# Optimization experiments

Hardware: AMD Instinct MI355X
Metric: run time of the kernel (lower is better)

The kernel has to match this reference:

```python
import jax, jax.numpy as jnp
import numpy as np

N = 100000      # nodes
E = 1600000     # edges
F_IN = 64       # num_node_features
HID = 128       # hidden_channels
HEADS = 8       # heads in gat1
G = 1000        # number of graphs
EPS = 1e-5


def _layer_norm(x, gamma, beta):
    mu = jnp.mean(x, axis=-1, keepdims=True)
    var = jnp.var(x, axis=-1, keepdims=True)
    return (x - mu) * jax.lax.rsqrt(var + EPS) * gamma + beta


def _gat_conv(x, src, dst, W, a_src, a_dst, b):
    # PyG GATConv (concat=True, negative_slope=0.2, self-loops already in src/dst)
    n = x.shape[0]
    heads, c = a_src.shape
    h = (x @ W).reshape(n, heads, c)                      # [N,H,C]
    alpha_s = jnp.sum(h * a_src[None], axis=-1)           # [N,H]
    alpha_d = jnp.sum(h * a_dst[None], axis=-1)           # [N,H]
    e = jax.nn.leaky_relu(alpha_s[src] + alpha_d[dst], 0.2)   # [Etot,H]
    m = jax.ops.segment_max(e, dst, num_segments=n)       # per-dst max (stable softmax)
    e = jnp.exp(e - m[dst])
    denom = jax.ops.segment_sum(e, dst, num_segments=n)
    attn = e / (denom[dst] + 1e-16)                        # [Etot,H]
    out = jax.ops.segment_sum(h[src] * attn[:, :, None], dst, num_segments=n)
    return out.reshape(n, heads * c) + b


def setup_inputs():
    key = jax.random.key(0)
    ks = jax.random.split(key, 32)
    s = 0.05
    inp = {
        'x': jax.random.normal(ks[0], (N, F_IN), dtype=jnp.float32),
        'edge_index': jax.random.randint(ks[1], (2, E), 0, N),
        'batch': jnp.sort(jax.random.randint(ks[2], (N,), 0, G)),
        # gat1: 64 -> 16 per head, 8 heads
        'W1': jax.random.normal(ks[3], (F_IN, HID), dtype=jnp.float32) * s,
        'as1': jax.random.normal(ks[4], (HEADS, HID // HEADS), dtype=jnp.float32) * s,
        'ad1': jax.random.normal(ks[5], (HEADS, HID // HEADS), dtype=jnp.float32) * s,
        'b1': jnp.zeros((HID,), dtype=jnp.float32),
        # gat2: 128 -> 128, 1 head
        'W2': jax.random.normal(ks[6], (HID, HID), dtype=jnp.float32) * s,
        'as2': jax.random.normal(ks[7], (1, HID), dtype=jnp.float32) * s,
        'ad2': jax.random.normal(ks[8], (1, HID), dtype=jnp.float32) * s,
        'b2': jnp.zeros((HID,), dtype=jnp.float32),
        # gat3
        'W3': jax.random.normal(ks[9], (HID, HID), dtype=jnp.float32) * s,
        'as3': jax.random.normal(ks[10], (1, HID), dtype=jnp.float32) * s,
        'ad3': jax.random.normal(ks[11], (1, HID), dtype=jnp.float32) * s,
        'b3': jnp.zeros((HID,), dtype=jnp.float32),
        # layer norms
        'g1': jnp.ones((HID,), dtype=jnp.float32), 'be1': jnp.zeros((HID,), dtype=jnp.float32),
        'g2': jnp.ones((HID,), dtype=jnp.float32), 'be2': jnp.zeros((HID,), dtype=jnp.float32),
        'g3': jnp.ones((HID,), dtype=jnp.float32), 'be3': jnp.zeros((HID,), dtype=jnp.float32),
        # linear heads
        'lw1': jax.random.normal(ks[12], (HID, HID), dtype=jnp.float32) * s,
        'lb1': jnp.zeros((HID,), dtype=jnp.float32),
        'lw2': jax.random.normal(ks[13], (HID, HID), dtype=jnp.float32) * s,
        'lb2': jnp.zeros((HID,), dtype=jnp.float32),
    }
    return inp


def reference(x, edge_index, batch, W1, as1, ad1, b1, W2, as2, ad2, b2,
              W3, as3, ad3, b3, g1, be1, g2, be2, g3, be3, lw1, lb1, lw2, lb2):
    n = x.shape[0]
    loops = jnp.arange(n)
    src = jnp.concatenate([edge_index[0], loops])   # add self-loops (PyG default)
    dst = jnp.concatenate([edge_index[1], loops])

    h = _gat_conv(x, src, dst, W1, as1, ad1, b1)
    h = _layer_norm(jax.nn.elu(h), g1, be1)          # dropout is identity in eval

    idn2 = h
    h = _gat_conv(h, src, dst, W2, as2, ad2, b2)
    h = _layer_norm(jax.nn.elu(h), g2, be2) + idn2

    idn3 = h
    h = _gat_conv(h, src, dst, W3, as3, ad3, b3)
    h = _layer_norm(jax.nn.elu(h), g3, be3) + idn3

    # global mean pool over graphs
    sums = jax.ops.segment_sum(h, batch, num_segments=G)
    cnt = jax.ops.segment_sum(jnp.ones((n, 1), h.dtype), batch, num_segments=G)
    pooled = sums / jnp.maximum(cnt, 1.0)

    out = jax.nn.elu(pooled @ lw1 + lb1)
    return out @ lw2 + lb2
```

## Files before the change

### kernel.cpp

```cpp
#include <hip/hip_runtime.h>
#include <hip/hip_bf16.h>
#include <cstdint>
#include <cstddef>

constexpr int F_IN = 64;
constexpr int HID  = 128;
constexpr int SCHUNK = 4096;

typedef __attribute__((ext_vector_type(8))) short short8v;
typedef __attribute__((ext_vector_type(4))) float f32x4;

__device__ __forceinline__ float bf2f(unsigned short u) {
  return __uint_as_float((unsigned)u << 16);
}
__device__ __forceinline__ unsigned short f2bf(float x) {
  unsigned u = __float_as_uint(x);
  u += 0x7FFFu + ((u >> 16) & 1u);
  return (unsigned short)(u >> 16);
}

__global__ __launch_bounds__(256) void k_bhist(const int* __restrict__ ei,
                                               int* __restrict__ bcnt, int E, int n) {
  __shared__ int hist[1024];
  int t = threadIdx.x;
  for (int k = t; k < 1024; k += 256) hist[k] = 0;
  __syncthreads();
  int tot = E + n;
  for (int i = blockIdx.x * 256 + t; i < tot; i += gridDim.x * 256) {
    int d = (i < E) ? ei[E + i] : (i - E);
    atomicAdd(&hist[d >> 7], 1);
  }
  __syncthreads();
  for (int k = t; k < 1024; k += 256)
    if (hist[k]) atomicAdd(&bcnt[k], hist[k]);
}

__global__ __launch_bounds__(1024) void k_bscan(const int* __restrict__ bcnt,
                                                int* __restrict__ boff,
                                                int* __restrict__ bcur, int nb) {
  __shared__ int tmp[1024];
  int t = threadIdx.x;
  int v = (t < nb) ? bcnt[t] : 0;
  tmp[t] = v;
  __syncthreads();
  #pragma unroll
  for (int off = 1; off < 1024; off <<= 1) {
    int x = tmp[t];
    int add = (t >= off) ? tmp[t - off] : 0;
    __syncthreads();
    tmp[t] = x + add;
    __syncthreads();
  }
  if (t < nb) {
    int ex = tmp[t] - v;
    boff[t] = ex;
    bcur[t] = ex;
    if (t == nb - 1) boff[nb] = tmp[t];
  }
}

__global__ __launch_bounds__(256) void k_bscat(const int* __restrict__ ei,
                                               int* __restrict__ bcur,
                                               uint2* __restrict__ pairs, int E, int n) {
  __shared__ int lh[1024];
  __shared__ int lc[1024];
  int t = threadIdx.x;
  int tot = E + n;
  int start = blockIdx.x * SCHUNK;
  if (start >= tot) return;
  int end = min(start + SCHUNK, tot);
  for (int k = t; k < 1024; k += 256) { lh[k] = 0; lc[k] = 0; }
  __syncthreads();
  int dreg[SCHUNK / 256];
  #pragma unroll
  for (int q = 0; q < SCHUNK / 256; ++q) {
    int i = start + q * 256 + t;
    int d = (i < end) ? ((i < E) ? ei[E + i] : (i - E)) : -1;
    dreg[q] = d;
    if (d >= 0) atomicAdd(&lh[d >> 7], 1);
  }
  __syncthreads();
  for (int k = t; k < 1024; k += 256) {
    int c = lh[k];
    lh[k] = (c > 0) ? atomicAdd(&bcur[k], c) : 0;
  }
  __syncthreads();
  #pragma unroll
  for (int q = 0; q < SCHUNK / 256; ++q) {
    int i = start + q * 256 + t;
    int d = dreg[q];
    if (d < 0) continue;
    int s = (i < E) ? ei[i] : (i - E);
    int b = d >> 7;
    int loc = atomicAdd(&lc[b], 1);
    pairs[lh[b] + loc] = make_uint2((unsigned)s, (unsigned)d);
  }
}

__global__ __launch_bounds__(256) void k_bfin(const uint2* __restrict__ pairs,
                                              const int* __restrict__ boff,
                                              int* __restrict__ row_off,
                                              int* __restrict__ csr_src,
                                              int n, int tot) {
  __shared__ int ldeg[128];
  __shared__ int lcur[128];
  int b = blockIdx.x;
  int t = threadIdx.x;
  int pb = boff[b], pe = boff[b + 1];
  if (t < 128) ldeg[t] = 0;
  __syncthreads();
  for (int j = pb + t; j < pe; j += 256)
    atomicAdd(&ldeg[pairs[j].y & 127], 1);
  __syncthreads();
  int cnt = (t < 128) ? ldeg[t] : 0;
  for (int off = 1; off < 128; off <<= 1) {
    int add = (t < 128 && t >= off) ? ldeg[t - off] : 0;
    __syncthreads();
    if (t < 128) ldeg[t] += add;
    __syncthreads();
  }
  if (t < 128) {
    int base = pb + ldeg[t] - cnt;
    lcur[t] = base;
    int idx = (b << 7) + t;
    if (idx < n) row_off[idx] = base;
  }
  if (b == 0 && t == 255) row_off[n] = tot;
  __syncthreads();
  for (int j = pb + t; j < pe; j += 256) {
    uint2 pr = pairs[j];
    int pos = atomicAdd(&lcur[pr.y & 127], 1);
    csr_src[pos] = (int)pr.x;
  }
}

__global__ void k_tobf(const float* __restrict__ X, unsigned short* __restrict__ Y,
                       int total) {
  int i = blockIdx.x * 256 + threadIdx.x;
  if (i < total) Y[i] = f2bf(X[i]);
}

__global__ void k_wpack(const float* __restrict__ W, unsigned short* __restrict__ Wf,
                        int K) {
  int i = blockIdx.x * 256 + threadIdx.x;
  int total = (K >> 5) * 4096;
  if (i >= total) return;
  int j    = i & 7;
  int lane = (i >> 3) & 63;
  int t    = (i >> 9) & 7;
  int ks   = i >> 12;
  int k = ks * 32 + (lane >> 4) * 8 + j;
  int c = t * 16 + (lane & 15);
  Wf[i] = f2bf(W[k * 128 + c]);
}

template<int K, int HEADS>
__global__ __launch_bounds__(256) void k_mgemm(const short* __restrict__ Xb,
                                               const short* __restrict__ Wf,
                                               const float* __restrict__ a_s,
                                               const float* __restrict__ a_d,
                                               unsigned short* __restrict__ Y,
                                               float* __restrict__ AS,
                                               float* __restrict__ AD, int n) {
  int wv   = threadIdx.x >> 6;
  int lane = threadIdx.x & 63;
  int r0   = blockIdx.x * 64 + wv * 16;
  int ln = lane & 15, kg = lane >> 4;
  f32x4 acc[8] = {};
  int arow = min(r0 + ln, n - 1);
  const short* aptr = Xb + arow * K + kg * 8;
  #pragma unroll
  for (int ks = 0; ks < K / 32; ++ks) {
    short8v a = *(const short8v*)(aptr + ks * 32);
    const short* wp = Wf + ks * 4096 + lane * 8;
    #pragma unroll
    for (int t = 0; t < 8; ++t) {
      short8v b = *(const short8v*)(wp + t * 512);
      acc[t] = __builtin_amdgcn_mfma_f32_16x16x32_bf16(a, b, acc[t], 0, 0, 0);
    }
  }
  float asv[8], adv[8];
  #pragma unroll
  for (int t = 0; t < 8; ++t) { asv[t] = a_s[t * 16 + ln]; adv[t] = a_d[t * 16 + ln]; }
  #pragma unroll
  for (int reg = 0; reg < 4; ++reg) {
    int r = r0 + kg * 4 + reg;
    bool valid = (r < n);
    if (HEADS == 1) {
      float s1 = 0.f, s2 = 0.f;
      #pragma unroll
      for (int t = 0; t < 8; ++t) {
        s1 = fmaf(acc[t][reg], asv[t], s1);
        s2 = fmaf(acc[t][reg], adv[t], s2);
      }
      #pragma unroll
      for (int off = 1; off < 16; off <<= 1) {
        s1 += __shfl_xor(s1, off);
        s2 += __shfl_xor(s2, off);
      }
      if (valid && ln == 0) { AS[r] = s1; AD[r] = s2; }
    } else {
      float s1[8], s2[8];
      #pragma unroll
      for (int t = 0; t < 8; ++t) {
        s1[t] = acc[t][reg] * asv[t];
        s2[t] = acc[t][reg] * adv[t];
      }
      #pragma unroll
      for (int off = 1; off < 16; off <<= 1) {
        #pragma unroll
        for (int t = 0; t < 8; ++t) {
          s1[t] += __shfl_xor(s1[t], off);
          s2[t] += __shfl_xor(s2[t], off);
        }
      }
      float w1 = s1[0], w2 = s2[0];
      #pragma unroll
      for (int t = 1; t < 8; ++t) {
        w1 = (ln == t) ? s1[t] : w1;
        w2 = (ln == t) ? s2[t] : w2;
      }
      if (valid && ln < 8) { AS[r * 8 + ln] = w1; AD[r * 8 + ln] = w2; }
    }
  }
  #pragma unroll
  for (int t = 0; t < 8; ++t) {
    #pragma unroll
    for (int reg = 0; reg < 4; ++reg) {
      int r = r0 + kg * 4 + reg;
      if (r < n) Y[r * 128 + t * 16 + ln] = f2bf(acc[t][reg]);
    }
  }
}

template<int LOGC>
__global__ __launch_bounds__(256) void k_agg_post(const unsigned short* __restrict__ Hu,
    const int* __restrict__ row_off, const int* __restrict__ csr_src,
    const float* __restrict__ AS, const float* __restrict__ AD,
    const float* __restrict__ bias, const unsigned short* __restrict__ RES,
    const float* __restrict__ gamma, const float* __restrict__ beta,
    unsigned short* __restrict__ Yb, int n, int has_res) {
  int tid = blockIdx.x * 256 + threadIdx.x;
  int wid = tid >> 5;
  int ll  = threadIdx.x & 31;
  if (wid >= n) return;
  constexpr int NH  = HID >> LOGC;
  constexpr int SEG = (LOGC >= 7) ? 32 : (1 << (LOGC - 2));
  int abslane = threadIdx.x & 63;
  int c = ll << 2;
  int h = c >> LOGC;
  int r = ll & (SEG - 1);
  int sbase = abslane & ~(SEG - 1);
  float adv = AD[wid * NH + h];
  int jb = row_off[wid], je = row_off[wid + 1];
  float den = 0.f, a0 = 0.f, a1 = 0.f, a2 = 0.f, a3 = 0.f;
  for (int j0 = jb; j0 < je; j0 += SEG) {
    int cnt = min(SEG, je - j0);
    int s_l = 0; float p_l = 0.f;
    if (r < cnt) {
      s_l = csr_src[j0 + r];
      float e = AS[s_l * NH + h] + adv;
      e = (e > 0.f) ? e : 0.2f * e;
      p_l = __expf(e);
    }
    int k = 0;
    if (LOGC >= 7) {
      for (; k + 8 <= cnt; k += 8) {
        int   sk[8]; float pk[8]; ushort4 uu[8];
        #pragma unroll
        for (int q = 0; q < 8; ++q) sk[q] = __shfl(s_l, sbase | (k + q));
        #pragma unroll
        for (int q = 0; q < 8; ++q) uu[q] = *(const ushort4*)(Hu + (sk[q] << 7) + c);
        #pragma unroll
        for (int q = 0; q < 8; ++q) pk[q] = __shfl(p_l, sbase | (k + q));
        #pragma unroll
        for (int q = 0; q < 8; ++q) {
          den += pk[q];
          a0 = fmaf(pk[q], bf2f(uu[q].x), a0);
          a1 = fmaf(pk[q], bf2f(uu[q].y), a1);
          a2 = fmaf(pk[q], bf2f(uu[q].z), a2);
          a3 = fmaf(pk[q], bf2f(uu[q].w), a3);
        }
      }
    }
    for (; k + 4 <= cnt; k += 4) {
      int sk0 = __shfl(s_l, sbase | k);
      int sk1 = __shfl(s_l, sbase | (k + 1));
      int sk2 = __shfl(s_l, sbase | (k + 2));
      int sk3 = __shfl(s_l, sbase | (k + 3));
      ushort4 u0 = *(const ushort4*)(Hu + (sk0 << 7) + c);
      ushort4 u1 = *(const ushort4*)(Hu + (sk1 << 7) + c);
      ushort4 u2 = *(const ushort4*)(Hu + (sk2 << 7) + c);
      ushort4 u3 = *(const ushort4*)(Hu + (sk3 << 7) + c);
      float p0 = __shfl(p_l, sbase | k);
      float p1 = __shfl(p_l, sbase | (k + 1));
      float p2 = __shfl(p_l, sbase | (k + 2));
      float p3 = __shfl(p_l, sbase | (k + 3));
      den += (p0 + p1) + (p2 + p3);
      a0 = fmaf(p0, bf2f(u0.x), a0); a1 = fmaf(p0, bf2f(u0.y), a1);
      a2 = fmaf(p0, bf2f(u0.z), a2); a3 = fmaf(p0, bf2f(u0.w), a3);
      a0 = fmaf(p1, bf2f(u1.x), a0); a1 = fmaf(p1, bf2f(u1.y), a1);
      a2 = fmaf(p1, bf2f(u1.z), a2); a3 = fmaf(p1, bf2f(u1.w), a3);
      a0 = fmaf(p2, bf2f(u2.x), a0); a1 = fmaf(p2, bf2f(u2.y), a1);
      a2 = fmaf(p2, bf2f(u2.z), a2); a3 = fmaf(p2, bf2f(u2.w), a3);
      a0 = fmaf(p3, bf2f(u3.x), a0); a1 = fmaf(p3, bf2f(u3.y), a1);
      a2 = fmaf(p3, bf2f(u3.z), a2); a3 = fmaf(p3, bf2f(u3.w), a3);
    }
    for (; k < cnt; ++k) {
      int   s  = __shfl(s_l, sbase | k);
      float pk = __shfl(p_l, sbase | k);
      ushort4 u = *(const ushort4*)(Hu + (s << 7) + c);
      den += pk;
      a0 = fmaf(pk, bf2f(u.x), a0); a1 = fmaf(pk, bf2f(u.y), a1);
      a2 = fmaf(pk, bf2f(u.z), a2); a3 = fmaf(pk, bf2f(u.w), a3);
    }
  }
  float inv = 1.f / (den + 1e-16f);
  float4 bv = *(const float4*)(bias + c);
  float t0 = a0 * inv + bv.x;
  float t1 = a1 * inv + bv.y;
  float t2 = a2 * inv + bv.z;
  float t3 = a3 * inv + bv.w;
  float e0 = t0 > 0.f ? t0 : __expf(t0) - 1.f;
  float e1 = t1 > 0.f ? t1 : __expf(t1) - 1.f;
  float e2 = t2 > 0.f ? t2 : __expf(t2) - 1.f;
  float e3 = t3 > 0.f ? t3 : __expf(t3) - 1.f;
  float s1 = (e0 + e1) + (e2 + e3);
  float s2 = (e0 * e0 + e1 * e1) + (e2 * e2 + e3 * e3);
  #pragma unroll
  for (int off = 16; off >= 1; off >>= 1) {
    s1 += __shfl_xor(s1, off);
    s2 += __shfl_xor(s2, off);
  }
  float mu  = s1 * (1.f / 128.f);
  float var = s2 * (1.f / 128.f) - mu * mu;
  float rs  = rsqrtf(var + 1e-5f);
  int base = wid * HID;
  float r0 = 0.f, r1 = 0.f, r2 = 0.f, r3 = 0.f;
  if (has_res) {
    ushort4 rv = *(const ushort4*)(RES + base + c);
    r0 = bf2f(rv.x); r1 = bf2f(rv.y); r2 = bf2f(rv.z); r3 = bf2f(rv.w);
  }
  float4 gv = *(const float4*)(gamma + c);
  float4 betv = *(const float4*)(beta + c);
  ushort4 ob;
  ob.x = f2bf((e0 - mu) * rs * gv.x + betv.x + r0);
  ob.y = f2bf((e1 - mu) * rs * gv.y + betv.y + r1);
  ob.z = f2bf((e2 - mu) * rs * gv.z + betv.z + r2);
  ob.w = f2bf((e3 - mu) * rs * gv.w + betv.w + r3);
  *(ushort4*)(Yb + base + c) = ob;
}

__global__ __launch_bounds__(256) void k_pool_seg(const unsigned short* __restrict__ Hf,
    const int* __restrict__ batch, float* __restrict__ pool, int n, int G) {
  int wid  = (int)((blockIdx.x * (size_t)blockDim.x + threadIdx.x) >> 6);
  int lane = threadIdx.x & 63;
  if (wid >= G) return;
  int lo = 0, hi = n;
  while (lo < hi) { int mid = (lo + hi) >> 1; if (batch[mid] < wid) lo = mid + 1; else hi = mid; }
  int start = lo;
  hi = n;
  while (lo < hi) { int mid = (lo + hi) >> 1; if (batch[mid] < wid + 1) lo = mid + 1; else hi = mid; }
  int end = lo;
  int c = 2 * lane;
  float s0 = 0.f, s1 = 0.f;
  for (int i = start; i < end; ++i) {
    ushort2 v = *(const ushort2*)(Hf + (size_t)i * HID + c);
    s0 += bf2f(v.x); s1 += bf2f(v.y);
  }
  float inv = 1.f / (float)max(end - start, 1);
  pool[(size_t)wid * HID + c]     = s0 * inv;
  pool[(size_t)wid * HID + c + 1] = s1 * inv;
}

__global__ void k_mlp(const float* __restrict__ X, const float* __restrict__ Wt,
                      const float* __restrict__ bb, float* __restrict__ Y,
                      int rows, int do_elu) {
  int i = blockIdx.x * blockDim.x + threadIdx.x;
  if (i >= rows * HID) return;
  int r = i >> 7, c = i & 127;
  const float* xr = X + (size_t)r * HID;
  float acc = bb[c];
  for (int k = 0; k < HID; ++k) acc += xr[k] * Wt[k * HID + c];
  if (do_elu) acc = acc > 0.f ? acc : __expf(acc) - 1.f;
  Y[i] = acc;
}

extern "C" void kernel_launch(void* const* d_in, const int* in_sizes, int n_in,
                              void* d_out, int out_size, void* d_ws, size_t ws_size,
                              hipStream_t stream) {
  const float* x   = (const float*)d_in[0];
  const int*   ei  = (const int*)d_in[1];
  const int*   bat = (const int*)d_in[2];
  const float* W1  = (const float*)d_in[3];
  const float* as1 = (const float*)d_in[4];
  const float* ad1 = (const float*)d_in[5];
  const float* b1  = (const float*)d_in[6];
  const float* W2  = (const float*)d_in[7];
  const float* as2 = (const float*)d_in[8];
  const float* ad2 = (const float*)d_in[9];
  const float* b2  = (const float*)d_in[10];
  const float* W3  = (const float*)d_in[11];
  const float* as3 = (const float*)d_in[12];
  const float* ad3 = (const float*)d_in[13];
  const float* b3  = (const float*)d_in[14];
  const float* g1  = (const float*)d_in[15];
  const float* be1 = (const float*)d_in[16];
  const float* g2  = (const float*)d_in[17];
  const float* be2 = (const float*)d_in[18];
  const float* g3  = (const float*)d_in[19];
  const float* be3 = (const float*)d_in[20];
  const float* lw1 = (const float*)d_in[21];
  const float* lb1 = (const float*)d_in[22];
  const float* lw2 = (const float*)d_in[23];
  const float* lb2 = (const float*)d_in[24];

  int N = in_sizes[0] / F_IN;
  int E = in_sizes[1] / 2;
  int G = out_size / HID;
  int tot = E + N;
  int nb  = (N + 127) >> 7;

  char* p = (char*)d_ws;
  auto alloc = [&](size_t bytes) { char* r = p; p += (bytes + 511) & ~(size_t)511; return r; };
  int*   bcnt    = (int*)  alloc(1024 * 4);
  int*   boff    = (int*)  alloc(1025 * 4);
  int*   bcur    = (int*)  alloc(1024 * 4);
  int*   row_off = (int*)  alloc((size_t)(N + 1) * 4);
  int*   csr_src = (int*)  alloc((size_t)tot * 4);
  uint2* pairs   = (uint2*)alloc((size_t)tot * 8);
  float* AS      = (float*)alloc((size_t)N * 8 * 4);
  float* AD      = (float*)alloc((size_t)N * 8 * 4);
  unsigned short* Hb  = (unsigned short*)alloc((size_t)N * HID * 2);
  unsigned short* Fb0 = (unsigned short*)alloc((size_t)N * HID * 2);
  unsigned short* Fb1 = (unsigned short*)alloc((size_t)N * HID * 2);
  unsigned short* Fb2 = (unsigned short*)alloc((size_t)N * HID * 2);
  float* pool    = (float*)alloc((size_t)G * HID * 4);
  float* t1      = (float*)alloc((size_t)G * HID * 4);
  unsigned short* Wf1 = (unsigned short*)alloc(64 * 128 * 2);
  unsigned short* Wf2 = (unsigned short*)alloc(128 * 128 * 2);
  unsigned short* Wf3 = (unsigned short*)alloc(128 * 128 * 2);
  unsigned short* xb  = (unsigned short*)pairs;

  (void)hipMemsetAsync(bcnt, 0, 1024 * 4, stream);

  int sb = (tot + SCHUNK - 1) / SCHUNK;
  k_bhist<<<256, 256, 0, stream>>>(ei, bcnt, E, N);
  k_bscan<<<1, 1024, 0, stream>>>(bcnt, boff, bcur, nb);
  k_bscat<<<sb, 256, 0, stream>>>(ei, bcur, pairs, E, N);
  k_bfin <<<nb, 256, 0, stream>>>(pairs, boff, row_off, csr_src, N, tot);

  k_tobf <<<(N * F_IN + 255) / 256, 256, 0, stream>>>(x, xb, N * F_IN);
  k_wpack<<<(64 * 128 + 255) / 256, 256, 0, stream>>>(W1, Wf1, 64);
  k_wpack<<<(128 * 128 + 255) / 256, 256, 0, stream>>>(W2, Wf2, 128);
  k_wpack<<<(128 * 128 + 255) / 256, 256, 0, stream>>>(W3, Wf3, 128);

  int mb  = (N + 63) / 64;
  int nh2 = (N + 7) / 8;

  k_mgemm<64, 8><<<mb, 256, 0, stream>>>((const short*)xb, (const short*)Wf1,
                                         as1, ad1, Hb, AS, AD, N);
  k_agg_post<4><<<nh2, 256, 0, stream>>>(Hb, row_off, csr_src, AS, AD, b1,
                                         nullptr, g1, be1, Fb0, N, 0);

  k_mgemm<128, 1><<<mb, 256, 0, stream>>>((const short*)Fb0, (const short*)Wf2,
                                          as2, ad2, Hb, AS, AD, N);
  k_agg_post<7><<<nh2, 256, 0, stream>>>(Hb, row_off, csr_src, AS, AD, b2,
                                         Fb0, g2, be2, Fb1, N, 1);

  k_mgemm<128, 1><<<mb, 256, 0, stream>>>((const short*)Fb1, (const short*)Wf3,
                                          as3, ad3, Hb, AS, AD, N);
  k_agg_post<7><<<nh2, 256, 0, stream>>>(Hb, row_off, csr_src, AS, AD, b3,
                                         Fb1, g3, be3, Fb2, N, 1);

  k_pool_seg<<<(G + 3) / 4, 256, 0, stream>>>(Fb2, bat, pool, N, G);
  k_mlp<<<(G * HID + 255) / 256, 256, 0, stream>>>(pool, lw1, lb1, t1, G, 1);
  k_mlp<<<(G * HID + 255) / 256, 256, 0, stream>>>(t1, lw2, lb2, (float*)d_out, G, 0);
}
```

Measured before the change: 420.0 us.

## Insert self-loops in CSR finalize, widen agg lanes, fuse prep and head kernels

Self-loop edges are no longer pushed through the histogram and scatter passes. The finalize kernel reserves one slot per node and writes the loop entry directly, which cuts scatter traffic and the size of the pairs buffer. The single-head aggregation now uses 16 lanes per node with 8-wide bf16 gathers instead of 32 lanes with 4-wide gathers. The float-to-bf16 conversion is vectorized, the three weight-pack launches become one, and pooling plus both MLP layers are fused into a single per-graph kernel. The changes reduce launch count and memory traffic, but each node now runs with fewer gather lanes.

New measurement: 429.5 us. 1.02x slower.

```diff
diff --git a/kernel.cpp b/kernel.cpp
--- a/kernel.cpp
+++ b/kernel.cpp
@@ -9,6 +9,7 @@
 
 typedef __attribute__((ext_vector_type(8))) short short8v;
 typedef __attribute__((ext_vector_type(4))) float f32x4;
+typedef __attribute__((ext_vector_type(8))) unsigned short ushort8v;
 
 __device__ __forceinline__ float bf2f(unsigned short u) {
   return __uint_as_float((unsigned)u << 16);
@@ -20,16 +21,13 @@
 }
 
 __global__ __launch_bounds__(256) void k_bhist(const int* __restrict__ ei,
-                                               int* __restrict__ bcnt, int E, int n) {
+                                               int* __restrict__ bcnt, int E) {
   __shared__ int hist[1024];
   int t = threadIdx.x;
   for (int k = t; k < 1024; k += 256) hist[k] = 0;
   __syncthreads();
-  int tot = E + n;
-  for (int i = blockIdx.x * 256 + t; i < tot; i += gridDim.x * 256) {
-    int d = (i < E) ? ei[E + i] : (i - E);
-    atomicAdd(&hist[d >> 7], 1);
-  }
+  for (int i = blockIdx.x * 256 + t; i < E; i += gridDim.x * 256)
+    atomicAdd(&hist[ei[E + i] >> 7], 1);
   __syncthreads();
   for (int k = t; k < 1024; k += 256)
     if (hist[k]) atomicAdd(&bcnt[k], hist[k]);
@@ -61,21 +59,20 @@
 
 __global__ __launch_bounds__(256) void k_bscat(const int* __restrict__ ei,
                                                int* __restrict__ bcur,
-                                               uint2* __restrict__ pairs, int E, int n) {
+                                               uint2* __restrict__ pairs, int E) {
   __shared__ int lh[1024];
   __shared__ int lc[1024];
   int t = threadIdx.x;
-  int tot = E + n;
   int start = blockIdx.x * SCHUNK;
-  if (start >= tot) return;
-  int end = min(start + SCHUNK, tot);
+  if (start >= E) return;
+  int end = min(start + SCHUNK, E);
   for (int k = t; k < 1024; k += 256) { lh[k] = 0; lc[k] = 0; }
   __syncthreads();
   int dreg[SCHUNK / 256];
   #pragma unroll
   for (int q = 0; q < SCHUNK / 256; ++q) {
     int i = start + q * 256 + t;
-    int d = (i < end) ? ((i < E) ? ei[E + i] : (i - E)) : -1;
+    int d = (i < end) ? ei[E + i] : -1;
     dreg[q] = d;
     if (d >= 0) atomicAdd(&lh[d >> 7], 1);
   }
@@ -90,7 +87,7 @@
     int i = start + q * 256 + t;
     int d = dreg[q];
     if (d < 0) continue;
-    int s = (i < E) ? ei[i] : (i - E);
+    int s = ei[i];
     int b = d >> 7;
     int loc = atomicAdd(&lc[b], 1);
     pairs[lh[b] + loc] = make_uint2((unsigned)s, (unsigned)d);
@@ -101,13 +98,15 @@
                                               const int* __restrict__ boff,
                                               int* __restrict__ row_off,
                                               int* __restrict__ csr_src,
-                                              int n, int tot) {
+                                              int n, int E) {
   __shared__ int ldeg[128];
   __shared__ int lcur[128];
   int b = blockIdx.x;
   int t = threadIdx.x;
   int pb = boff[b], pe = boff[b + 1];
-  if (t < 128) ldeg[t] = 0;
+  int fullbase = pb + min(b << 7, n);
+  int idx = (b << 7) + t;
+  if (t < 128) ldeg[t] = (idx < n) ? 1 : 0;
   __syncthreads();
   for (int j = pb + t; j < pe; j += 256)
     atomicAdd(&ldeg[pairs[j].y & 127], 1);
@@ -120,12 +119,14 @@
     __syncthreads();
   }
   if (t < 128) {
-    int base = pb + ldeg[t] - cnt;
-    lcur[t] = base;
-    int idx = (b << 7) + t;
-    if (idx < n) row_off[idx] = base;
-  }
-  if (b == 0 && t == 255) row_off[n] = tot;
+    int base = fullbase + ldeg[t] - cnt;
+    if (idx < n) {
+      row_off[idx] = base;
+      csr_src[base] = idx;
+      lcur[t] = base + 1;
+    } else lcur[t] = base;
+  }
+  if (b == 0 && t == 255) row_off[n] = E + n;
   __syncthreads();
   for (int j = pb + t; j < pe; j += 256) {
     uint2 pr = pairs[j];
@@ -134,24 +135,32 @@
   }
 }
 
-__global__ void k_tobf(const float* __restrict__ X, unsigned short* __restrict__ Y,
-                       int total) {
+__global__ void k_tobf4(const float4* __restrict__ X, ushort4* __restrict__ Y,
+                        int total4) {
   int i = blockIdx.x * 256 + threadIdx.x;
-  if (i < total) Y[i] = f2bf(X[i]);
-}
-
-__global__ void k_wpack(const float* __restrict__ W, unsigned short* __restrict__ Wf,
-                        int K) {
+  if (i >= total4) return;
+  float4 v = X[i];
+  ushort4 o;
+  o.x = f2bf(v.x); o.y = f2bf(v.y); o.z = f2bf(v.z); o.w = f2bf(v.w);
+  Y[i] = o;
+}
+
+__global__ void k_wpack3(const float* __restrict__ W1, const float* __restrict__ W2,
+                         const float* __restrict__ W3, unsigned short* __restrict__ Wf1,
+                         unsigned short* __restrict__ Wf2, unsigned short* __restrict__ Wf3) {
   int i = blockIdx.x * 256 + threadIdx.x;
-  int total = (K >> 5) * 4096;
-  if (i >= total) return;
-  int j    = i & 7;
-  int lane = (i >> 3) & 63;
-  int t    = (i >> 9) & 7;
-  int ks   = i >> 12;
+  const float* W; unsigned short* Wf; int idx;
+  if (i < 8192)       { W = W1; Wf = Wf1; idx = i; }
+  else if (i < 24576) { W = W2; Wf = Wf2; idx = i - 8192; }
+  else if (i < 40960) { W = W3; Wf = Wf3; idx = i - 24576; }
+  else return;
+  int j    = idx & 7;
+  int lane = (idx >> 3) & 63;
+  int t    = (idx >> 9) & 7;
+  int ks   = idx >> 12;
   int k = ks * 32 + (lane >> 4) * 8 + j;
   int c = t * 16 + (lane & 15);
-  Wf[i] = f2bf(W[k * 128 + c]);
+  Wf[idx] = f2bf(W[k * 128 + c]);
 }
 
 template<int K, int HEADS>
@@ -240,150 +249,209 @@
     const float* __restrict__ bias, const unsigned short* __restrict__ RES,
     const float* __restrict__ gamma, const float* __restrict__ beta,
     unsigned short* __restrict__ Yb, int n, int has_res) {
-  int tid = blockIdx.x * 256 + threadIdx.x;
-  int wid = tid >> 5;
-  int ll  = threadIdx.x & 31;
-  if (wid >= n) return;
-  constexpr int NH  = HID >> LOGC;
-  constexpr int SEG = (LOGC >= 7) ? 32 : (1 << (LOGC - 2));
-  int abslane = threadIdx.x & 63;
-  int c = ll << 2;
-  int h = c >> LOGC;
-  int r = ll & (SEG - 1);
-  int sbase = abslane & ~(SEG - 1);
-  float adv = AD[wid * NH + h];
-  int jb = row_off[wid], je = row_off[wid + 1];
-  float den = 0.f, a0 = 0.f, a1 = 0.f, a2 = 0.f, a3 = 0.f;
-  for (int j0 = jb; j0 < je; j0 += SEG) {
-    int cnt = min(SEG, je - j0);
-    int s_l = 0; float p_l = 0.f;
-    if (r < cnt) {
-      s_l = csr_src[j0 + r];
-      float e = AS[s_l * NH + h] + adv;
-      e = (e > 0.f) ? e : 0.2f * e;
-      p_l = __expf(e);
-    }
-    int k = 0;
-    if (LOGC >= 7) {
+  if constexpr (LOGC >= 7) {
+    int tid = blockIdx.x * 256 + threadIdx.x;
+    int wid = tid >> 4;
+    int ll  = threadIdx.x & 15;
+    if (wid >= n) return;
+    int c = ll << 3;
+    int sbase = (threadIdx.x & 63) & ~15;
+    float adv = AD[wid];
+    int jb = row_off[wid], je = row_off[wid + 1];
+    float den = 0.f, a[8] = {};
+    for (int j0 = jb; j0 < je; j0 += 16) {
+      int cnt = min(16, je - j0);
+      int s_l = 0; float p_l = 0.f;
+      if (ll < cnt) {
+        s_l = csr_src[j0 + ll];
+        float e = AS[s_l] + adv;
+        e = (e > 0.f) ? e : 0.2f * e;
+        p_l = __expf(e);
+      }
+      int k = 0;
       for (; k + 8 <= cnt; k += 8) {
-        int   sk[8]; float pk[8]; ushort4 uu[8];
+        int sk[8]; float pk[8]; ushort8v uu[8];
         #pragma unroll
         for (int q = 0; q < 8; ++q) sk[q] = __shfl(s_l, sbase | (k + q));
         #pragma unroll
-        for (int q = 0; q < 8; ++q) uu[q] = *(const ushort4*)(Hu + (sk[q] << 7) + c);
+        for (int q = 0; q < 8; ++q) uu[q] = *(const ushort8v*)(Hu + (sk[q] << 7) + c);
         #pragma unroll
         for (int q = 0; q < 8; ++q) pk[q] = __shfl(p_l, sbase | (k + q));
         #pragma unroll
         for (int q = 0; q < 8; ++q) {
           den += pk[q];
-          a0 = fmaf(pk[q], bf2f(uu[q].x), a0);
-          a1 = fmaf(pk[q], bf2f(uu[q].y), a1);
-          a2 = fmaf(pk[q], bf2f(uu[q].z), a2);
-          a3 = fmaf(pk[q], bf2f(uu[q].w), a3);
+          #pragma unroll
+          for (int m = 0; m < 8; ++m) a[m] = fmaf(pk[q], bf2f(uu[q][m]), a[m]);
         }
       }
-    }
-    for (; k + 4 <= cnt; k += 4) {
-      int sk0 = __shfl(s_l, sbase | k);
-      int sk1 = __shfl(s_l, sbase | (k + 1));
-      int sk2 = __shfl(s_l, sbase | (k + 2));
-      int sk3 = __shfl(s_l, sbase | (k + 3));
-      ushort4 u0 = *(const ushort4*)(Hu + (sk0 << 7) + c);
-      ushort4 u1 = *(const ushort4*)(Hu + (sk1 << 7) + c);
-      ushort4 u2 = *(const ushort4*)(Hu + (sk2 << 7) + c);
-      ushort4 u3 = *(const ushort4*)(Hu + (sk3 << 7) + c);
-      float p0 = __shfl(p_l, sbase | k);
-      float p1 = __shfl(p_l, sbase | (k + 1));
-      float p2 = __shfl(p_l, sbase | (k + 2));
-      float p3 = __shfl(p_l, sbase | (k + 3));
-      den += (p0 + p1) + (p2 + p3);
-      a0 = fmaf(p0, bf2f(u0.x), a0); a1 = fmaf(p0, bf2f(u0.y), a1);
-      a2 = fmaf(p0, bf2f(u0.z), a2); a3 = fmaf(p0, bf2f(u0.w), a3);
-      a0 = fmaf(p1, bf2f(u1.x), a0); a1 = fmaf(p1, bf2f(u1.y), a1);
-      a2 = fmaf(p1, bf2f(u1.z), a2); a3 = fmaf(p1, bf2f(u1.w), a3);
-      a0 = fmaf(p2, bf2f(u2.x), a0); a1 = fmaf(p2, bf2f(u2.y), a1);
-      a2 = fmaf(p2, bf2f(u2.z), a2); a3 = fmaf(p2, bf2f(u2.w), a3);
-      a0 = fmaf(p3, bf2f(u3.x), a0); a1 = fmaf(p3, bf2f(u3.y), a1);
-      a2 = fmaf(p3, bf2f(u3.z), a2); a3 = fmaf(p3, bf2f(u3.w), a3);
-    }
-    for (; k < cnt; ++k) {
-      int   s  = __shfl(s_l, sbase | k);
-      float pk = __shfl(p_l, sbase | k);
-      ushort4 u = *(const ushort4*)(Hu + (s << 7) + c);
-      den += pk;
-      a0 = fmaf(pk, bf2f(u.x), a0); a1 = fmaf(pk, bf2f(u.y), a1);
-      a2 = fmaf(pk, bf2f(u.z), a2); a3 = fmaf(pk, bf2f(u.w), a3);
-    }
-  }
-  float inv = 1.f / (den + 1e-16f);
-  float4 bv = *(const float4*)(bias + c);
-  float t0 = a0 * inv + bv.x;
-  float t1 = a1 * inv + bv.y;
-  float t2 = a2 * inv + bv.z;
-  float t3 = a3 * inv + bv.w;
-  float e0 = t0 > 0.f ? t0 : __expf(t0) - 1.f;
-  float e1 = t1 > 0.f ? t1 : __expf(t1) - 1.f;
-  float e2 = t2 > 0.f ? t2 : __expf(t2) - 1.f;
-  float e3 = t3 > 0.f ? t3 : __expf(t3) - 1.f;
-  float s1 = (e0 + e1) + (e2 + e3);
-  float s2 = (e0 * e0 + e1 * e1) + (e2 * e2 + e3 * e3);
-  #pragma unroll
-  for (int off = 16; off >= 1; off >>= 1) {
-    s1 += __shfl_xor(s1, off);
-    s2 += __shfl_xor(s2, off);
-  }
-  float mu  = s1 * (1.f / 128.f);
-  float var = s2 * (1.f / 128.f) - mu * mu;
-  float rs  = rsqrtf(var + 1e-5f);
-  int base = wid * HID;
-  float r0 = 0.f, r1 = 0.f, r2 = 0.f, r3 = 0.f;
-  if (has_res) {
-    ushort4 rv = *(const ushort4*)(RES + base + c);
-    r0 = bf2f(rv.x); r1 = bf2f(rv.y); r2 = bf2f(rv.z); r3 = bf2f(rv.w);
-  }
-  float4 gv = *(const float4*)(gamma + c);
-  float4 betv = *(const float4*)(beta + c);
-  ushort4 ob;
-  ob.x = f2bf((e0 - mu) * rs * gv.x + betv.x + r0);
-  ob.y = f2bf((e1 - mu) * rs * gv.y + betv.y + r1);
-  ob.z = f2bf((e2 - mu) * rs * gv.z + betv.z + r2);
-  ob.w = f2bf((e3 - mu) * rs * gv.w + betv.w + r3);
-  *(ushort4*)(Yb + base + c) = ob;
-}
-
-__global__ __launch_bounds__(256) void k_pool_seg(const unsigned short* __restrict__ Hf,
-    const int* __restrict__ batch, float* __restrict__ pool, int n, int G) {
-  int wid  = (int)((blockIdx.x * (size_t)blockDim.x + threadIdx.x) >> 6);
-  int lane = threadIdx.x & 63;
-  if (wid >= G) return;
+      for (; k < cnt; ++k) {
+        int   s  = __shfl(s_l, sbase | k);
+        float pk = __shfl(p_l, sbase | k);
+        ushort8v u = *(const ushort8v*)(Hu + (s << 7) + c);
+        den += pk;
+        #pragma unroll
+        for (int m = 0; m < 8; ++m) a[m] = fmaf(pk, bf2f(u[m]), a[m]);
+      }
+    }
+    float inv = 1.f / (den + 1e-16f);
+    float4 bv0 = *(const float4*)(bias + c);
+    float4 bv1 = *(const float4*)(bias + c + 4);
+    float e[8];
+    float bb[8] = {bv0.x, bv0.y, bv0.z, bv0.w, bv1.x, bv1.y, bv1.z, bv1.w};
+    #pragma unroll
+    for (int m = 0; m < 8; ++m) {
+      float t = a[m] * inv + bb[m];
+      e[m] = t > 0.f ? t : __expf(t) - 1.f;
+    }
+    float s1 = 0.f, s2 = 0.f;
+    #pragma unroll
+    for (int m = 0; m < 8; ++m) { s1 += e[m]; s2 += e[m] * e[m]; }
+    #pragma unroll
+    for (int off = 1; off < 16; off <<= 1) {
+      s1 += __shfl_xor(s1, off);
+      s2 += __shfl_xor(s2, off);
+    }
+    float mu  = s1 * (1.f / 128.f);
+    float var = s2 * (1.f / 128.f) - mu * mu;
+    float rs  = rsqrtf(var + 1e-5f);
+    int base = wid * HID;
+    float rr[8] = {};
+    if (has_res) {
+      ushort8v rv = *(const ushort8v*)(RES + base + c);
+      #pragma unroll
+      for (int m = 0; m < 8; ++m) rr[m] = bf2f(rv[m]);
+    }
+    float4 gv0 = *(const float4*)(gamma + c);
+    float4 gv1 = *(const float4*)(gamma + c + 4);
+    float4 tv0 = *(const float4*)(beta + c);
+    float4 tv1 = *(const float4*)(beta + c + 4);
+    float gg[8] = {gv0.x, gv0.y, gv0.z, gv0.w, gv1.x, gv1.y, gv1.z, gv1.w};
+    float tt[8] = {tv0.x, tv0.y, tv0.z, tv0.w, tv1.x, tv1.y, tv1.z, tv1.w};
+    ushort8v ob;
+    #pragma unroll
+    for (int m = 0; m < 8; ++m) ob[m] = f2bf((e[m] - mu) * rs * gg[m] + tt[m] + rr[m]);
+    *(ushort8v*)(Yb + base + c) = ob;
+  } else {
+    int tid = blockIdx.x * 256 + threadIdx.x;
+    int wid = tid >> 5;
+    int ll  = threadIdx.x & 31;
+    if (wid >= n) return;
+    constexpr int NH  = HID >> LOGC;
+    constexpr int SEG = 1 << (LOGC - 2);
+    int abslane = threadIdx.x & 63;
+    int c = ll << 2;
+    int h = c >> LOGC;
+    int r = ll & (SEG - 1);
+    int sbase = abslane & ~(SEG - 1);
+    float adv = AD[wid * NH + h];
+    int jb = row_off[wid], je = row_off[wid + 1];
+    float den = 0.f, a0 = 0.f, a1 = 0.f, a2 = 0.f, a3 = 0.f;
+    for (int j0 = jb; j0 < je; j0 += SEG) {
+      int cnt = min(SEG, je - j0);
+      int s_l = 0; float p_l = 0.f;
+      if (r < cnt) {
+        s_l = csr_src[j0 + r];
+        float e = AS[s_l * NH + h] + adv;
+        e = (e > 0.f) ? e : 0.2f * e;
+        p_l = __expf(e);
+      }
+      int k = 0;
+      for (; k + 4 <= cnt; k += 4) {
+        int sk0 = __shfl(s_l, sbase | k);
+        int sk1 = __shfl(s_l, sbase | (k + 1));
+        int sk2 = __shfl(s_l, sbase | (k + 2));
+        int sk3 = __shfl(s_l, sbase | (k + 3));
+        ushort4 u0 = *(const ushort4*)(Hu + (sk0 << 7) + c);
+        ushort4 u1 = *(const ushort4*)(Hu + (sk1 << 7) + c);
+        ushort4 u2 = *(const ushort4*)(Hu + (sk2 << 7) + c);
+        ushort4 u3 = *(const ushort4*)(Hu + (sk3 << 7) + c);
+        float p0 = __shfl(p_l, sbase | k);
+        float p1 = __shfl(p_l, sbase | (k + 1));
+        float p2 = __shfl(p_l, sbase | (k + 2));
+        float p3 = __shfl(p_l, sbase | (k + 3));
+        den += (p0 + p1) + (p2 + p3);
+        a0 = fmaf(p0, bf2f(u0.x), a0); a1 = fmaf(p0, bf2f(u0.y), a1);
+        a2 = fmaf(p0, bf2f(u0.z), a2); a3 = fmaf(p0, bf2f(u0.w), a3);
+        a0 = fmaf(p1, bf2f(u1.x), a0); a1 = fmaf(p1, bf2f(u1.y), a1);
+        a2 = fmaf(p1, bf2f(u1.z), a2); a3 = fmaf(p1, bf2f(u1.w), a3);
+        a0 = fmaf(p2, bf2f(u2.x), a0); a1 = fmaf(p2, bf2f(u2.y), a1);
+        a2 = fmaf(p2, bf2f(u2.z), a2); a3 = fmaf(p2, bf2f(u2.w), a3);
+        a0 = fmaf(p3, bf2f(u3.x), a0); a1 = fmaf(p3, bf2f(u3.y), a1);
+        a2 = fmaf(p3, bf2f(u3.z), a2); a3 = fmaf(p3, bf2f(u3.w), a3);
+      }
+      for (; k < cnt; ++k) {
+        int   s  = __shfl(s_l, sbase | k);
+        float pk = __shfl(p_l, sbase | k);
+        ushort4 u = *(const ushort4*)(Hu + (s << 7) + c);
+        den += pk;
+        a0 = fmaf(pk, bf2f(u.x), a0); a1 = fmaf(pk, bf2f(u.y), a1);
+        a2 = fmaf(pk, bf2f(u.z), a2); a3 = fmaf(pk, bf2f(u.w), a3);
+      }
+    }
+    float inv = 1.f / (den + 1e-16f);
+    float4 bv = *(const float4*)(bias + c);
+    float t0 = a0 * inv + bv.x;
+    float t1 = a1 * inv + bv.y;
+    float t2 = a2 * inv + bv.z;
+    float t3 = a3 * inv + bv.w;
+    float e0 = t0 > 0.f ? t0 : __expf(t0) - 1.f;
+    float e1 = t1 > 0.f ? t1 : __expf(t1) - 1.f;
+    float e2 = t2 > 0.f ? t2 : __expf(t2) - 1.f;
+    float e3 = t3 > 0.f ? t3 : __expf(t3) - 1.f;
+    float s1 = (e0 + e1) + (e2 + e3);
+    float s2 = (e0 * e0 + e1 * e1) + (e2 * e2 + e3 * e3);
+    #pragma unroll
+    for (int off = 16; off >= 1; off >>= 1) {
+      s1 += __shfl_xor(s1, off);
+      s2 += __shfl_xor(s2, off);
+    }
+    float mu  = s1 * (1.f / 128.f);
+    float var = s2 * (1.f / 128.f) - mu * mu;
+    float rs  = rsqrtf(var + 1e-5f);
+    int base = wid * HID;
+    float r0 = 0.f, r1 = 0.f, r2 = 0.f, r3 = 0.f;
+    if (has_res) {
+      ushort4 rv = *(const ushort4*)(RES + base + c);
+      r0 = bf2f(rv.x); r1 = bf2f(rv.y); r2 = bf2f(rv.z); r3 = bf2f(rv.w);
+    }
+    float4 gv = *(const float4*)(gamma + c);
+    float4 betv = *(const float4*)(beta + c);
+    ushort4 ob;
+    ob.x = f2bf((e0 - mu) * rs * gv.x + betv.x + r0);
+    ob.y = f2bf((e1 - mu) * rs * gv.y + betv.y + r1);
+    ob.z = f2bf((e2 - mu) * rs * gv.z + betv.z + r2);
+    ob.w = f2bf((e3 - mu) * rs * gv.w + betv.w + r3);
+    *(ushort4*)(Yb + base + c) = ob;
+  }
+}
+
+__global__ __launch_bounds__(128) void k_head(const unsigned short* __restrict__ Hf,
+    const int* __restrict__ batch, const float* __restrict__ lw1,
+    const float* __restrict__ lb1, const float* __restrict__ lw2,
+    const float* __restrict__ lb2, float* __restrict__ out, int n) {
+  __shared__ float pooled[128];
+  __shared__ float h1[128];
+  int g = blockIdx.x;
+  int c = threadIdx.x;
   int lo = 0, hi = n;
-  while (lo < hi) { int mid = (lo + hi) >> 1; if (batch[mid] < wid) lo = mid + 1; else hi = mid; }
+  while (lo < hi) { int mid = (lo + hi) >> 1; if (batch[mid] < g) lo = mid + 1; else hi = mid; }
   int start = lo;
   hi = n;
-  while (lo < hi) { int mid = (lo + hi) >> 1; if (batch[mid] < wid + 1) lo = mid + 1; else hi = mid; }
+  while (lo < hi) { int mid = (lo + hi) >> 1; if (batch[mid] < g + 1) lo = mid + 1; else hi = mid; }
   int end = lo;
-  int c = 2 * lane;
-  float s0 = 0.f, s1 = 0.f;
-  for (int i = start; i < end; ++i) {
-    ushort2 v = *(const ushort2*)(Hf + (size_t)i * HID + c);
-    s0 += bf2f(v.x); s1 += bf2f(v.y);
-  }
-  float inv = 1.f / (float)max(end - start, 1);
-  pool[(size_t)wid * HID + c]     = s0 * inv;
-  pool[(size_t)wid * HID + c + 1] = s1 * inv;
-}
-
-__global__ void k_mlp(const float* __restrict__ X, const float* __restrict__ Wt,
-                      const float* __restrict__ bb, float* __restrict__ Y,
-                      int rows, int do_elu) {
-  int i = blockIdx.x * blockDim.x + threadIdx.x;
-  if (i >= rows * HID) return;
-  int r = i >> 7, c = i & 127;
-  const float* xr = X + (size_t)r * HID;
-  float acc = bb[c];
-  for (int k = 0; k < HID; ++k) acc += xr[k] * Wt[k * HID + c];
-  if (do_elu) acc = acc > 0.f ? acc : __expf(acc) - 1.f;
-  Y[i] = acc;
+  float s = 0.f;
+  for (int i = start; i < end; ++i) s += bf2f(Hf[(size_t)i * 128 + c]);
+  pooled[c] = s / (float)max(end - start, 1);
+  __syncthreads();
+  float acc = lb1[c];
+  #pragma unroll 8
+  for (int k = 0; k < 128; ++k) acc = fmaf(pooled[k], lw1[k * 128 + c], acc);
+  h1[c] = acc > 0.f ? acc : __expf(acc) - 1.f;
+  __syncthreads();
+  float acc2 = lb2[c];
+  #pragma unroll 8
+  for (int k = 0; k < 128; ++k) acc2 = fmaf(h1[k], lw2[k * 128 + c], acc2);
+  out[(size_t)g * 128 + c] = acc2;
 }
 
 extern "C" void kernel_launch(void* const* d_in, const int* in_sizes, int n_in,
@@ -428,15 +496,13 @@
   int*   bcur    = (int*)  alloc(1024 * 4);
   int*   row_off = (int*)  alloc((size_t)(N + 1) * 4);
   int*   csr_src = (int*)  alloc((size_t)tot * 4);
-  uint2* pairs   = (uint2*)alloc((size_t)tot * 8);
+  uint2* pairs   = (uint2*)alloc((size_t)E * 8);
   float* AS      = (float*)alloc((size_t)N * 8 * 4);
   float* AD      = (float*)alloc((size_t)N * 8 * 4);
   unsigned short* Hb  = (unsigned short*)alloc((size_t)N * HID * 2);
   unsigned short* Fb0 = (unsigned short*)alloc((size_t)N * HID * 2);
   unsigned short* Fb1 = (unsigned short*)alloc((size_t)N * HID * 2);
   unsigned short* Fb2 = (unsigned short*)alloc((size_t)N * HID * 2);
-  float* pool    = (float*)alloc((size_t)G * HID * 4);
-  float* t1      = (float*)alloc((size_t)G * HID * 4);
   unsigned short* Wf1 = (unsigned short*)alloc(64 * 128 * 2);
   unsigned short* Wf2 = (unsigned short*)alloc(128 * 128 * 2);
   unsigned short* Wf3 = (unsigned short*)alloc(128 * 128 * 2);
@@ -444,36 +510,34 @@
 
   (void)hipMemsetAsync(bcnt, 0, 1024 * 4, stream);
 
-  int sb = (tot + SCHUNK - 1) / SCHUNK;
-  k_bhist<<<256, 256, 0, stream>>>(ei, bcnt, E, N);
+  int sb = (E + SCHUNK - 1) / SCHUNK;
+  k_bhist<<<256, 256, 0, stream>>>(ei, bcnt, E);
   k_bscan<<<1, 1024, 0, stream>>>(bcnt, boff, bcur, nb);
-  k_bscat<<<sb, 256, 0, stream>>>(ei, bcur, pairs, E, N);
-  k_bfin <<<nb, 256, 0, stream>>>(pairs, boff, row_off, csr_src, N, tot);
-
-  k_tobf <<<(N * F_IN + 255) / 256, 256, 0, stream>>>(x, xb, N * F_IN);
-  k_wpack<<<(64 * 128 + 255) / 256, 256, 0, stream>>>(W1, Wf1, 64);
-  k_wpack<<<(128 * 128 + 255) / 256, 256, 0, stream>>>(W2, Wf2, 128);
-  k_wpack<<<(128 * 128 + 255) / 256, 256, 0, stream>>>(W3, Wf3, 128);
+  k_bscat<<<sb, 256, 0, stream>>>(ei, bcur, pairs, E);
+  k_bfin <<<nb, 256, 0, stream>>>(pairs, boff, row_off, csr_src, N, E);
+
+  k_tobf4 <<<(N * F_IN / 4 + 255) / 256, 256, 0, stream>>>((const float4*)x,
+                                                           (ushort4*)xb, N * F_IN / 4);
+  k_wpack3<<<160, 256, 0, stream>>>(W1, W2, W3, Wf1, Wf2, Wf3);
 
   int mb  = (N + 63) / 64;
-  int nh2 = (N + 7) / 8;
+  int nh4 = (N + 7) / 8;
+  int nh7 = (N + 15) / 16;
 
   k_mgemm<64, 8><<<mb, 256, 0, stream>>>((const short*)xb, (const short*)Wf1,
                                          as1, ad1, Hb, AS, AD, N);
-  k_agg_post<4><<<nh2, 256, 0, stream>>>(Hb, row_off, csr_src, AS, AD, b1,
+  k_agg_post<4><<<nh4, 256, 0, stream>>>(Hb, row_off, csr_src, AS, AD, b1,
                                          nullptr, g1, be1, Fb0, N, 0);
 
   k_mgemm<128, 1><<<mb, 256, 0, stream>>>((const short*)Fb0, (const short*)Wf2,
                                           as2, ad2, Hb, AS, AD, N);
-  k_agg_post<7><<<nh2, 256, 0, stream>>>(Hb, row_off, csr_src, AS, AD, b2,
+  k_agg_post<7><<<nh7, 256, 0, stream>>>(Hb, row_off, csr_src, AS, AD, b2,
                                          Fb0, g2, be2, Fb1, N, 1);
 
   k_mgemm<128, 1><<<mb, 256, 0, stream>>>((const short*)Fb1, (const short*)Wf3,
                                           as3, ad3, Hb, AS, AD, N);
-  k_agg_post<7><<<nh2, 256, 0, stream>>>(Hb, row_off, csr_src, AS, AD, b3,
+  k_agg_post<7><<<nh7, 256, 0, stream>>>(Hb, row_off, csr_src, AS, AD, b3,
                                          Fb1, g3, be3, Fb2, N, 1);
 
-  k_pool_seg<<<(G + 3) / 4, 256, 0, stream>>>(Fb2, bat, pool, N, G);
-  k_mlp<<<(G * HID + 255) / 256, 256, 0, stream>>>(pool, lw1, lb1, t1, G, 1);
-  k_mlp<<<(G * HID + 255) / 256, 256, 0, stream>>>(t1, lw2, lb2, (float*)d_out, G, 0);
-}
+  k_head<<<G, 128, 0, stream>>>(Fb2, bat, lw1, lb1, lw2, lb2, (float*)d_out, N);
+}
```
